# Optimization experiments

Hardware: AMD Instinct MI355X
Metric: run time of the kernel (lower is better)

The kernel has to match this reference:

```python
import jax, jax.numpy as jnp
import numpy as np

D_MODEL = 1024
BASE = 7
NUM_PLANES = 2
EPS = 1e-6


def setup_inputs() -> dict:
    key = jax.random.key(0)
    k_x, k_w, k_t, k_g = jax.random.split(key, 4)
    B, S, D = 4, 8192, D_MODEL
    x = jax.random.normal(k_x, (B, S, D), dtype=jnp.float32)
    # eidosTransform params: linear 3D -> D, then 2 planes of learned rotation angles over D/2 pairs
    W = jax.random.normal(k_w, (3 * D, D), dtype=jnp.float32) / np.sqrt(3 * D)
    b = jnp.zeros((D,), dtype=jnp.float32)
    theta = jax.random.normal(k_t, (NUM_PLANES, D // 2), dtype=jnp.float32) * 0.1
    # ModularPhaseNorm gain
    gamma = jnp.ones((D,), dtype=jnp.float32)
    return {"x": x, "W": W, "b": b, "theta": theta, "gamma": gamma}


def _eidos_transform(t, W, b, theta):
    # linear projection 3D -> D ('truncate' collapse to d_out)
    y = jnp.einsum("bse,ed->bsd", t, W) + b  # [B,S,D]
    B, S, D = y.shape
    # geometric mode: rotate (even, odd) dim pairs by learned angles, per plane
    for p in range(NUM_PLANES):
        yp = y.reshape(B, S, D // 2, 2)
        a, c2 = yp[..., 0], yp[..., 1]
        cos_t = jnp.cos(theta[p])
        sin_t = jnp.sin(theta[p])
        ra = a * cos_t - c2 * sin_t
        rb = a * sin_t + c2 * cos_t
        y = jnp.stack([ra, rb], axis=-1).reshape(B, S, D)
    return y


def _modular_phase_norm(y, gamma):
    # RMS-normalize within feature groups defined by (dim index mod BASE)
    D = y.shape[-1]
    group = jnp.arange(D) % BASE                      # [D]
    onehot = jax.nn.one_hot(group, BASE, dtype=y.dtype)  # [D, BASE]
    counts = onehot.sum(axis=0)                       # [BASE]
    ss = jnp.einsum("bsd,dg->bsg", y * y, onehot)     # [B,S,BASE]
    rms = jnp.sqrt(ss / counts + EPS)                 # [B,S,BASE]
    denom = rms[..., group]                           # [B,S,D]
    return y / denom * gamma


def reference(x, W, b, theta, gamma):
    B, S, D = x.shape
    zero_row = jnp.zeros((B, 1, D), dtype=x.dtype)
    left = jnp.concatenate([zero_row, x[:, :-1, :]], axis=1)   # roll +1, zero first
    right = jnp.concatenate([x[:, 1:, :], zero_row], axis=1)   # roll -1, zero last
    triplet = jnp.concatenate([left, x, right], axis=-1)        # [B,S,3D]
    mixed = _eidos_transform(triplet, W, b, theta)
    return _modular_phase_norm(mixed, gamma)
```

## Files before the change

### kernel.cpp

```cpp
#include <hip/hip_runtime.h>
#include <hip/hip_bf16.h>
#include <stdint.h>


#define SEQ 8192
#define NB 4
#define DM 1024
#define KD 3072

typedef __attribute__((ext_vector_type(8))) short short8_t;
typedef __attribute__((ext_vector_type(4))) float f32x4;

__device__ __forceinline__ unsigned short f2bf(float f) {
  union { float f; uint32_t u; } v; v.f = f;
  return (unsigned short)((v.u + 0x7fffu + ((v.u >> 16) & 1u)) >> 16);
}

__device__ __forceinline__ void async_ld16(const void* g, void* l) {
  __builtin_amdgcn_global_load_lds(
      (const __attribute__((address_space(1))) uint32_t*)g,
      (__attribute__((address_space(3))) uint32_t*)(uint32_t)(uintptr_t)l,
      16, 0, 0);
}

__global__ __launch_bounds__(256) void prep_w(const float* __restrict__ W,
                                              const float* __restrict__ theta,
                                              unsigned short* __restrict__ Wt) {
  __shared__ float csc[32], css[32];
  __shared__ unsigned short tile[64][72];
  const int bk = blockIdx.x % 48, bn = blockIdx.x / 48;
  const int k0 = bk * 64, n0 = bn * 64;
  const int t = threadIdx.x;
  if (t < 32) {
    int d = n0 / 2 + t;
    float ang = theta[d] + theta[512 + d];
    csc[t] = cosf(ang); css[t] = sinf(ang);
  }
  __syncthreads();
#pragma unroll
  for (int i = 0; i < 8; ++i) {
    int idx = i * 256 + t;
    int pr = idx >> 5;
    int pc = idx & 31;
    const float2 w2 = *(const float2*)&W[(size_t)(k0 + pr) * DM + n0 + pc * 2];
    float c = csc[pc], s = css[pc];
    tile[pc * 2][pr]     = f2bf(w2.x * c - w2.y * s);
    tile[pc * 2 + 1][pr] = f2bf(w2.x * s + w2.y * c);
  }
  __syncthreads();
#pragma unroll
  for (int i = 0; i < 16; ++i) {
    int idx = i * 256 + t;
    int r = idx >> 6, cdx = idx & 63;
    Wt[(size_t)(n0 + r) * KD + k0 + cdx] = tile[r][cdx];
  }
}

__global__ void prep_bias(const float* __restrict__ b, const float* __restrict__ theta,
                          float* __restrict__ biasp, float* __restrict__ zp) {
  const int t = threadIdx.x;
  float ang = theta[t] + theta[512 + t];
  float c = cosf(ang), s = sinf(ang);
  float be = b[2 * t], bo = b[2 * t + 1];
  biasp[2 * t]     = be * c - bo * s;
  biasp[2 * t + 1] = be * s + bo * c;
  if (t < 256) ((float4*)zp)[t] = make_float4(0.f, 0.f, 0.f, 0.f);
}

__global__ __launch_bounds__(256) void prep_x(const float* __restrict__ x,
                                              unsigned short* __restrict__ xbp) {
  const size_t total = (size_t)NB * 8194 * 128;
  for (size_t i = (size_t)blockIdx.x * 256 + threadIdx.x; i < total;
       i += (size_t)gridDim.x * 256) {
    int d8 = (int)(i & 127);
    size_t rem = i >> 7;
    int sp = (int)(rem % 8194);
    size_t bb = rem / 8194;
    uint4 o = make_uint4(0u, 0u, 0u, 0u);
    if (sp > 0 && sp < 8193) {
      const float4* src = (const float4*)(x + (bb * SEQ + (size_t)(sp - 1)) * DM + d8 * 8);
      float4 lo = src[0], hi = src[1];
      o.x = (uint32_t)f2bf(lo.x) | ((uint32_t)f2bf(lo.y) << 16);
      o.y = (uint32_t)f2bf(lo.z) | ((uint32_t)f2bf(lo.w) << 16);
      o.z = (uint32_t)f2bf(hi.x) | ((uint32_t)f2bf(hi.y) << 16);
      o.w = (uint32_t)f2bf(hi.z) | ((uint32_t)f2bf(hi.w) << 16);
    }
    ((uint4*)xbp)[i] = o;
  }
}

template <int AFP32>
__global__ __launch_bounds__(256) void gemm_kernel(const void* __restrict__ Ag,
                                                   const unsigned short* __restrict__ Wt,
                                                   const float* __restrict__ biasp,
                                                   const float* __restrict__ zp,
                                                   float* __restrict__ out) {
  constexpr int ABYTES = AFP32 ? 128 * 64 * 4 : 128 * 64 * 2;
  __shared__ __align__(16) unsigned char As[ABYTES];
  __shared__ __align__(16) unsigned char Bs[128 * 64 * 2];

  const int tid = threadIdx.x;
  const int lane = tid & 63;
  const int wid = tid >> 6;
  const int wm = wid >> 1, wn = wid & 1;
  const int row16 = lane & 15, kgrp = lane >> 4;

  const int L = blockIdx.x;
  const int xcd = L & 7;
  const int j = L >> 3;
  const int mtile = xcd * 32 + (j >> 3);
  const int ntile = j & 7;

  const int n0 = ntile * 128;
  const int batch = mtile >> 6;
  const int s0 = (mtile & 63) * 128;
  const size_t m0 = (size_t)mtile * 128;

  f32x4 acc[4][4];
#pragma unroll
  for (int a = 0; a < 4; ++a)
#pragma unroll
    for (int b = 0; b < 4; ++b) acc[a][b] = (f32x4){0.f, 0.f, 0.f, 0.f};

  for (int kt = 0; kt < 48; ++kt) {
    const int c = kt >> 4;
    const int ksb = (kt & 15) * 64;
    __syncthreads();
    if constexpr (!AFP32) {
#pragma unroll
      for (int it = 0; it < 4; ++it) {
        int f16 = it * 256 + tid;
        int row = f16 >> 3, c16 = f16 & 7;
        int c16s = c16 ^ (row & 7);
        const unsigned short* src = (const unsigned short*)Ag +
            ((size_t)batch * 8194 + (size_t)(s0 + row + c)) * DM + ksb + c16s * 8;
        async_ld16(src, As + f16 * 16);
      }
    } else {
#pragma unroll
      for (int it = 0; it < 8; ++it) {
        int f16 = it * 256 + tid;
        int row = f16 >> 4, c16 = f16 & 15;
        int c16s = c16 ^ (row & 7);
        int s = s0 + row + c - 1;
        const float* src = (s >= 0 && s < SEQ)
            ? (const float*)Ag + ((size_t)batch * SEQ + (size_t)s) * DM + ksb + c16s * 4
            : zp + c16s * 4;
        async_ld16(src, As + f16 * 16);
      }
    }
#pragma unroll
    for (int it = 0; it < 4; ++it) {
      int f16 = it * 256 + tid;
      int row = f16 >> 3, c16 = f16 & 7;
      int c16s = c16 ^ (row & 7);
      const unsigned short* src = Wt + (size_t)(n0 + row) * KD + kt * 64 + c16s * 8;
      async_ld16(src, Bs + f16 * 16);
    }
    __syncthreads();

#pragma unroll
    for (int kk = 0; kk < 2; ++kk) {
      short8_t af[4], bfr[4];
#pragma unroll
      for (int mi = 0; mi < 4; ++mi) {
        int r = wm * 64 + mi * 16 + row16;
        if constexpr (!AFP32) {
          int kb = kk * 64 + kgrp * 16;
          af[mi] = *(const short8_t*)(As + r * 128 + (kb ^ ((r & 7) << 4)));
        } else {
          int kb = kk * 128 + kgrp * 32;
          f32x4 lo = *(const f32x4*)(As + r * 256 + (kb ^ ((r & 7) << 4)));
          f32x4 hi = *(const f32x4*)(As + r * 256 + ((kb + 16) ^ ((r & 7) << 4)));
          union { short8_t v; unsigned short u[8]; } pk;
          pk.u[0] = f2bf(lo[0]); pk.u[1] = f2bf(lo[1]);
          pk.u[2] = f2bf(lo[2]); pk.u[3] = f2bf(lo[3]);
          pk.u[4] = f2bf(hi[0]); pk.u[5] = f2bf(hi[1]);
          pk.u[6] = f2bf(hi[2]); pk.u[7] = f2bf(hi[3]);
          af[mi] = pk.v;
        }
      }
#pragma unroll
      for (int ni = 0; ni < 4; ++ni) {
        int r = wn * 64 + ni * 16 + row16;
        int kb = kk * 64 + kgrp * 16;
        bfr[ni] = *(const short8_t*)(Bs + r * 128 + (kb ^ ((r & 7) << 4)));
      }
#pragma unroll
      for (int mi = 0; mi < 4; ++mi)
#pragma unroll
        for (int ni = 0; ni < 4; ++ni)
          acc[mi][ni] = __builtin_amdgcn_mfma_f32_16x16x32_bf16(
              af[mi], bfr[ni], acc[mi][ni], 0, 0, 0);
    }
  }

#pragma unroll
  for (int mi = 0; mi < 4; ++mi) {
    size_t grow = m0 + (size_t)(wm * 64 + mi * 16 + kgrp * 4);
#pragma unroll
    for (int ni = 0; ni < 4; ++ni) {
      int col = n0 + wn * 64 + ni * 16 + row16;
      float bia = biasp[col];
      float* op = out + grow * DM + col;
#pragma unroll
      for (int r = 0; r < 4; ++r) op[(size_t)r * DM] = acc[mi][ni][r] + bia;
    }
  }
}

__global__ __launch_bounds__(256) void norm_kernel(float* __restrict__ y,
                                                   const float* __restrict__ gamma) {
  const int tid = threadIdx.x, lane = tid & 63, wv = tid >> 6;
  const size_t row = (size_t)blockIdx.x * 4 + wv;
  float4* rp = (float4*)(y + row * DM);
  const float4* gp = (const float4*)gamma;
  float4 v[4];
#pragma unroll
  for (int jj = 0; jj < 4; ++jj) v[jj] = rp[jj * 64 + lane];

  float ss[7] = {0.f, 0.f, 0.f, 0.f, 0.f, 0.f, 0.f};
#pragma unroll
  for (int jj = 0; jj < 4; ++jj) {
    const float vv[4] = {v[jj].x, v[jj].y, v[jj].z, v[jj].w};
#pragma unroll
    for (int i = 0; i < 4; ++i) {
      int d = (jj * 64 + lane) * 4 + i;
      int g = d % 7;
      float sq = vv[i] * vv[i];
#pragma unroll
      for (int t = 0; t < 7; ++t) ss[t] += (g == t) ? sq : 0.f;
    }
  }
#pragma unroll
  for (int t = 0; t < 7; ++t) {
#pragma unroll
    for (int off = 32; off >= 1; off >>= 1) ss[t] += __shfl_xor(ss[t], off, 64);
  }
  float inv[7];
#pragma unroll
  for (int t = 0; t < 7; ++t) {
    float cnt = (t < 2) ? 147.f : 146.f;
    inv[t] = rsqrtf(ss[t] / cnt + 1e-6f);
  }
#pragma unroll
  for (int jj = 0; jj < 4; ++jj) {
    float4 g4 = gp[jj * 64 + lane];
    const float vv[4] = {v[jj].x, v[jj].y, v[jj].z, v[jj].w};
    const float gg[4] = {g4.x, g4.y, g4.z, g4.w};
    float o[4];
#pragma unroll
    for (int i = 0; i < 4; ++i) {
      int d = (jj * 64 + lane) * 4 + i;
      int g = d % 7;
      float iv = inv[0];
#pragma unroll
      for (int t = 1; t < 7; ++t) iv = (g == t) ? inv[t] : iv;
      o[i] = vv[i] * iv * gg[i];
    }
    rp[jj * 64 + lane] = make_float4(o[0], o[1], o[2], o[3]);
  }
}

extern "C" void kernel_launch(void* const* d_in, const int* in_sizes, int n_in,
                              void* d_out, int out_size, void* d_ws, size_t ws_size,
                              hipStream_t stream) {
  const float* x     = (const float*)d_in[0];
  const float* W     = (const float*)d_in[1];
  const float* b     = (const float*)d_in[2];
  const float* theta = (const float*)d_in[3];
  const float* gamma = (const float*)d_in[4];
  float* out = (float*)d_out;
  (void)in_sizes; (void)n_in; (void)out_size;

  char* ws = (char*)d_ws;
  unsigned short* Wt = (unsigned short*)ws;
  float* biasp = (float*)(ws + 6291456);
  float* zp    = (float*)(ws + 6291456 + 4096);
  unsigned short* xbp = (unsigned short*)(ws + 6299648);
  const size_t needA = 6299648 + (size_t)NB * 8194 * DM * 2;

  prep_w<<<dim3(768), dim3(256), 0, stream>>>(W, theta, Wt);
  prep_bias<<<dim3(1), dim3(512), 0, stream>>>(b, theta, biasp, zp);

  if (ws_size >= needA) {
    prep_x<<<dim3(4096), dim3(256), 0, stream>>>(x, xbp);
    gemm_kernel<0><<<dim3(2048), dim3(256), 0, stream>>>(
        (const void*)xbp, Wt, biasp, zp, out);
  } else {
    gemm_kernel<1><<<dim3(2048), dim3(256), 0, stream>>>(
        (const void*)x, Wt, biasp, zp, out);
  }
  norm_kernel<<<dim3(8192), dim3(256), 0, stream>>>(out, gamma);
}
```

Baseline: 314.1 us.

## Replace bf16 GEMM with 256x256-tile kernel using 4-stage async LDS pipeline

Replaces the 128x128-tile, single-buffered bf16 GEMM with a 512-thread kernel that computes 256x256 tiles over K-steps of 32. Loads are issued three stages ahead into a 4-deep LDS ring, with explicit vmcnt waits, barriers and raised MFMA priority. The aim is to overlap global loads with MFMA work and to raise data reuse per tile. The costs are that the new kernel uses 128KB of LDS, drops the XOR swizzle on LDS rows so bank conflicts may appear, launches only 512 blocks, and relies on hand-tuned waitcnt logic. The fp32 fallback path becomes a separate kernel with unchanged behaviour.

```diff
diff --git a/kernel.cpp b/kernel.cpp
--- a/kernel.cpp
+++ b/kernel.cpp
@@ -89,14 +89,130 @@
   }
 }
 
-template <int AFP32>
-__global__ __launch_bounds__(256) void gemm_kernel(const void* __restrict__ Ag,
-                                                   const unsigned short* __restrict__ Wt,
-                                                   const float* __restrict__ biasp,
-                                                   const float* __restrict__ zp,
-                                                   float* __restrict__ out) {
-  constexpr int ABYTES = AFP32 ? 128 * 64 * 4 : 128 * 64 * 2;
-  __shared__ __align__(16) unsigned char As[ABYTES];
+__global__ __launch_bounds__(512, 2) void gemm256(const unsigned short* __restrict__ xbp,
+                                                  const unsigned short* __restrict__ Wt,
+                                                  const float* __restrict__ biasp,
+                                                  float* __restrict__ out) {
+  __shared__ __align__(16) unsigned char As[4][16384];
+  __shared__ __align__(16) unsigned char Bs[4][16384];
+
+  const int tid = threadIdx.x;
+  const int lane = tid & 63;
+  const int wid = tid >> 6;
+  const int wm = wid >> 2, wn = wid & 3;
+  const int row16 = lane & 15, kgrp = lane >> 4;
+
+  const int L = blockIdx.x;
+  const int xcd = L & 7;
+  const int j = L >> 3;
+  const int mtile = xcd * 16 + (j >> 2);
+  const int ntile = j & 3;
+
+  const int n0 = ntile * 256;
+  const int batch = mtile >> 5;
+  const int s0 = (mtile & 31) * 256;
+  const size_t m0 = (size_t)mtile * 256;
+
+  auto stageA = [&](int kt, int buf) {
+    const int c = kt >> 5;
+    const int ksb = (kt & 31) * 32;
+    const size_t base = ((size_t)batch * 8194 + (size_t)(s0 + c)) * DM + ksb;
+#pragma unroll
+    for (int i = 0; i < 2; ++i) {
+      int idx = i * 512 + tid;
+      int row = idx >> 2, c16 = idx & 3;
+      async_ld16(xbp + base + (size_t)row * DM + c16 * 8, &As[buf][idx * 16]);
+    }
+  };
+  auto stageB = [&](int kt, int buf) {
+    const int kb = kt * 32;
+#pragma unroll
+    for (int i = 0; i < 2; ++i) {
+      int idx = i * 512 + tid;
+      int row = idx >> 2, c16 = idx & 3;
+      async_ld16(Wt + (size_t)(n0 + row) * KD + kb + c16 * 8, &Bs[buf][idx * 16]);
+    }
+  };
+
+  f32x4 acc[8][4];
+#pragma unroll
+  for (int a = 0; a < 8; ++a)
+#pragma unroll
+    for (int b = 0; b < 4; ++b) acc[a][b] = (f32x4){0.f, 0.f, 0.f, 0.f};
+
+  stageA(0, 0); stageB(0, 0);
+  stageA(1, 1); stageB(1, 1);
+  stageA(2, 2); stageB(2, 2);
+  asm volatile("s_waitcnt vmcnt(8)" ::: "memory");
+  __builtin_amdgcn_s_barrier();
+
+  for (int kt = 0; kt < 96; ++kt) {
+    const int buf = kt & 3, sbuf = (kt + 3) & 3;
+    const unsigned char* Ab = As[buf];
+    const unsigned char* Bb = Bs[buf];
+    short8_t af[4], bf[4];
+
+#pragma unroll
+    for (int mi = 0; mi < 4; ++mi)
+      af[mi] = *(const short8_t*)(Ab + (wm * 128 + mi * 16 + row16) * 64 + kgrp * 16);
+#pragma unroll
+    for (int ni = 0; ni < 4; ++ni)
+      bf[ni] = *(const short8_t*)(Bb + (wn * 64 + ni * 16 + row16) * 64 + kgrp * 16);
+    if (kt < 93) stageA(kt + 3, sbuf);
+    __builtin_amdgcn_s_barrier();
+    asm volatile("s_waitcnt lgkmcnt(0)" ::: "memory");
+    __builtin_amdgcn_sched_barrier(0);
+    __builtin_amdgcn_s_setprio(1);
+#pragma unroll
+    for (int mi = 0; mi < 4; ++mi)
+#pragma unroll
+      for (int ni = 0; ni < 4; ++ni)
+        acc[mi][ni] = __builtin_amdgcn_mfma_f32_16x16x32_bf16(
+            af[mi], bf[ni], acc[mi][ni], 0, 0, 0);
+    __builtin_amdgcn_s_setprio(0);
+    __builtin_amdgcn_s_barrier();
+
+#pragma unroll
+    for (int mi = 0; mi < 4; ++mi)
+      af[mi] = *(const short8_t*)(Ab + (wm * 128 + 64 + mi * 16 + row16) * 64 + kgrp * 16);
+    if (kt < 93) stageB(kt + 3, sbuf);
+    __builtin_amdgcn_s_barrier();
+    asm volatile("s_waitcnt lgkmcnt(0)" ::: "memory");
+    __builtin_amdgcn_sched_barrier(0);
+    __builtin_amdgcn_s_setprio(1);
+#pragma unroll
+    for (int mi = 0; mi < 4; ++mi)
+#pragma unroll
+      for (int ni = 0; ni < 4; ++ni)
+        acc[mi + 4][ni] = __builtin_amdgcn_mfma_f32_16x16x32_bf16(
+            af[mi], bf[ni], acc[mi + 4][ni], 0, 0, 0);
+    __builtin_amdgcn_s_setprio(0);
+    if (kt < 93)      asm volatile("s_waitcnt vmcnt(8)" ::: "memory");
+    else if (kt == 93) asm volatile("s_waitcnt vmcnt(4)" ::: "memory");
+    else if (kt == 94) asm volatile("s_waitcnt vmcnt(0)" ::: "memory");
+    __builtin_amdgcn_s_barrier();
+  }
+
+#pragma unroll
+  for (int mi = 0; mi < 8; ++mi) {
+    size_t grow = m0 + (size_t)(wm * 128 + mi * 16 + kgrp * 4);
+#pragma unroll
+    for (int ni = 0; ni < 4; ++ni) {
+      int col = n0 + wn * 64 + ni * 16 + row16;
+      float bia = biasp[col];
+      float* op = out + grow * DM + col;
+#pragma unroll
+      for (int r = 0; r < 4; ++r) op[(size_t)r * DM] = acc[mi][ni][r] + bia;
+    }
+  }
+}
+
+__global__ __launch_bounds__(256) void gemm_fb(const float* __restrict__ Ag,
+                                               const unsigned short* __restrict__ Wt,
+                                               const float* __restrict__ biasp,
+                                               const float* __restrict__ zp,
+                                               float* __restrict__ out) {
+  __shared__ __align__(16) unsigned char As[128 * 64 * 4];
   __shared__ __align__(16) unsigned char Bs[128 * 64 * 2];
 
   const int tid = threadIdx.x;
@@ -126,28 +242,16 @@
     const int c = kt >> 4;
     const int ksb = (kt & 15) * 64;
     __syncthreads();
-    if constexpr (!AFP32) {
-#pragma unroll
-      for (int it = 0; it < 4; ++it) {
-        int f16 = it * 256 + tid;
-        int row = f16 >> 3, c16 = f16 & 7;
-        int c16s = c16 ^ (row & 7);
-        const unsigned short* src = (const unsigned short*)Ag +
-            ((size_t)batch * 8194 + (size_t)(s0 + row + c)) * DM + ksb + c16s * 8;
-        async_ld16(src, As + f16 * 16);
-      }
-    } else {
-#pragma unroll
-      for (int it = 0; it < 8; ++it) {
-        int f16 = it * 256 + tid;
-        int row = f16 >> 4, c16 = f16 & 15;
-        int c16s = c16 ^ (row & 7);
-        int s = s0 + row + c - 1;
-        const float* src = (s >= 0 && s < SEQ)
-            ? (const float*)Ag + ((size_t)batch * SEQ + (size_t)s) * DM + ksb + c16s * 4
-            : zp + c16s * 4;
-        async_ld16(src, As + f16 * 16);
-      }
+#pragma unroll
+    for (int it = 0; it < 8; ++it) {
+      int f16 = it * 256 + tid;
+      int row = f16 >> 4, c16 = f16 & 15;
+      int c16s = c16 ^ (row & 7);
+      int s = s0 + row + c - 1;
+      const float* src = (s >= 0 && s < SEQ)
+          ? Ag + ((size_t)batch * SEQ + (size_t)s) * DM + ksb + c16s * 4
+          : zp + c16s * 4;
+      async_ld16(src, As + f16 * 16);
     }
 #pragma unroll
     for (int it = 0; it < 4; ++it) {
@@ -165,20 +269,15 @@
 #pragma unroll
       for (int mi = 0; mi < 4; ++mi) {
         int r = wm * 64 + mi * 16 + row16;
-        if constexpr (!AFP32) {
-          int kb = kk * 64 + kgrp * 16;
-          af[mi] = *(const short8_t*)(As + r * 128 + (kb ^ ((r & 7) << 4)));
-        } else {
-          int kb = kk * 128 + kgrp * 32;
-          f32x4 lo = *(const f32x4*)(As + r * 256 + (kb ^ ((r & 7) << 4)));
-          f32x4 hi = *(const f32x4*)(As + r * 256 + ((kb + 16) ^ ((r & 7) << 4)));
-          union { short8_t v; unsigned short u[8]; } pk;
-          pk.u[0] = f2bf(lo[0]); pk.u[1] = f2bf(lo[1]);
-          pk.u[2] = f2bf(lo[2]); pk.u[3] = f2bf(lo[3]);
-          pk.u[4] = f2bf(hi[0]); pk.u[5] = f2bf(hi[1]);
-          pk.u[6] = f2bf(hi[2]); pk.u[7] = f2bf(hi[3]);
-          af[mi] = pk.v;
-        }
+        int kb = kk * 128 + kgrp * 32;
+        f32x4 lo = *(const f32x4*)(As + r * 256 + (kb ^ ((r & 7) << 4)));
+        f32x4 hi = *(const f32x4*)(As + r * 256 + ((kb + 16) ^ ((r & 7) << 4)));
+        union { short8_t v; unsigned short u[8]; } pk;
+        pk.u[0] = f2bf(lo[0]); pk.u[1] = f2bf(lo[1]);
+        pk.u[2] = f2bf(lo[2]); pk.u[3] = f2bf(lo[3]);
+        pk.u[4] = f2bf(hi[0]); pk.u[5] = f2bf(hi[1]);
+        pk.u[6] = f2bf(hi[2]); pk.u[7] = f2bf(hi[3]);
+        af[mi] = pk.v;
       }
 #pragma unroll
       for (int ni = 0; ni < 4; ++ni) {
@@ -285,11 +384,9 @@
 
   if (ws_size >= needA) {
     prep_x<<<dim3(4096), dim3(256), 0, stream>>>(x, xbp);
-    gemm_kernel<0><<<dim3(2048), dim3(256), 0, stream>>>(
-        (const void*)xbp, Wt, biasp, zp, out);
+    gemm256<<<dim3(512), dim3(512), 0, stream>>>(xbp, Wt, biasp, out);
   } else {
-    gemm_kernel<1><<<dim3(2048), dim3(256), 0, stream>>>(
-        (const void*)x, Wt, biasp, zp, out);
+    gemm_fb<<<dim3(2048), dim3(256), 0, stream>>>(x, Wt, biasp, zp, out);
   }
   norm_kernel<<<dim3(8192), dim3(256), 0, stream>>>(out, gamma);
 }
```

After: 281.9 us. 10.2% less time.
